# Kernel tuning notes

Hardware: AMD Instinct MI355X
Metric: run time of the kernel (lower is better)

The kernel has to match this reference:

```python
import jax, jax.numpy as jnp
import numpy as np

N = 120000
CIN = 64
C = 128
H = 8
FF = 1.0          # focusing_factor
EPS = 1e-4
BN_EPS = 1e-3
LN_EPS = 1e-3
GX, GY, GZ = 160, 160, 40  # voxel grid for generating realistic sparse coords


def _bn(x, g, b, m, v):
    # inference-mode BatchNorm1d
    return (x - m) * jax.lax.rsqrt(v + BN_EPS) * g + b


def _ln(x, g, b):
    mu = jnp.mean(x, axis=-1, keepdims=True)
    var = jnp.mean(jnp.square(x - mu), axis=-1, keepdims=True)
    return (x - mu) * jax.lax.rsqrt(var + LN_EPS) * g + b


def _l2(x):
    return jnp.sqrt(jnp.sum(jnp.square(x), axis=-1, keepdims=True))


def _forward(features, indices, nbr, W_pre, b_pre, g_pre, be_pre, m_pre, v_pre,
             Wp1, bp1, g_pe, be_pe, m_pe, v_pe, Wp2, bp2,
             W_qkv, b_qkv, scale_p, W_dwc, b_dwc, W_proj, b_proj, g_n1, b_n1):
    sp = _bn(features @ W_pre + b_pre, g_pre, be_pre, m_pre, v_pre)      # [N,C]
    xyz = indices[:, 1:].astype(sp.dtype)                                # [N,3]
    pe = jax.nn.relu(_bn(xyz @ Wp1 + bp1, g_pe, be_pe, m_pe, v_pe)) @ Wp2 + bp2
    qkv = (sp @ W_qkv + b_qkv).reshape(-1, 3, C)
    q, k, v = qkv[:, 0], qkv[:, 1], qkv[:, 2]
    k = k + pe
    # kernel feature map: ReLU + eps
    q = jax.nn.relu(q) + EPS
    k = jax.nn.relu(k) + EPS
    scale = jax.nn.softplus(scale_p)
    q = q / scale
    k = k / scale
    qn, kn = _l2(q), _l2(k)
    # power-law focusing (focusing_factor <= 6 branch)
    q = q ** FF
    k = k ** FF
    # L2 renormalization back to original norms
    q = q / _l2(q) * qn
    k = k / _l2(k) * kn
    d = C // H
    q = q.reshape(-1, H, d).transpose(1, 0, 2)   # [H,N,d]
    k = k.reshape(-1, H, d).transpose(1, 0, 2)
    v = v.reshape(-1, H, d).transpose(1, 0, 2)
    i = j = q.shape[1]
    z = 1.0 / (jnp.einsum('hic,hc->hi', q, k.sum(axis=1)) + EPS)         # [H,N]
    if i * j * (d + d) > d * d * (i + j):
        kv = jnp.einsum('hjc,hjd->hcd', k, v)                            # [H,d,d]
        x = jnp.einsum('hic,hcd->hid', q, kv) * z[..., None]
    else:
        qk = jnp.einsum('hic,hjc->hij', q, k)
        x = jnp.einsum('hij,hjd->hid', qk, v) * z[..., None]
    x = x.transpose(1, 0, 2).reshape(-1, C)                              # [N,C]
    v_full = v.transpose(1, 0, 2).reshape(-1, C)
    # SubMConv3d(C, C, 3) on v via precomputed neighbor table nbr [N,27] (-1 = absent)
    conv = jnp.zeros_like(x)
    nmax = v_full.shape[0] - 1
    for t in range(27):
        idx = nbr[:, t]
        g = jnp.where((idx >= 0)[:, None], v_full[jnp.clip(idx, 0, nmax)], 0.0)
        conv = conv + g @ W_dwc[t]
    conv = conv + b_dwc
    x = x + conv
    x = x @ W_proj + b_proj
    x = _ln(x + sp, g_n1, b_n1)
    return x


def setup_inputs() -> dict:
    rng = np.random.default_rng(0)
    total = GX * GY * GZ
    lin = rng.choice(total, size=N, replace=False)
    x = lin // (GY * GZ)
    rem = lin % (GY * GZ)
    y = rem // GZ
    z = rem % GZ
    dense = -np.ones(total, dtype=np.int32)
    dense[lin] = np.arange(N, dtype=np.int32)
    cols = []
    for dx in (-1, 0, 1):
        for dy in (-1, 0, 1):
            for dz in (-1, 0, 1):
                nx, ny, nz = x + dx, y + dy, z + dz
                valid = (nx >= 0) & (nx < GX) & (ny >= 0) & (ny < GY) & (nz >= 0) & (nz < GZ)
                nlin = np.clip(nx * GY * GZ + ny * GZ + nz, 0, total - 1)
                cols.append(np.where(valid, dense[nlin], -1).astype(np.int32))
    nbr = np.stack(cols, axis=1)
    indices = np.stack([np.zeros(N, dtype=np.int32), x.astype(np.int32),
                        y.astype(np.int32), z.astype(np.int32)], axis=1)
    key = jax.random.key(0)
    ks = jax.random.split(key, 10)
    rn = lambda k, shape, s=0.05: jax.random.normal(k, shape, jnp.float32) * s
    return {
        'features': jax.random.normal(ks[0], (N, CIN), jnp.float32),
        'indices': jnp.asarray(indices),
        'nbr': jnp.asarray(nbr),
        'W_pre': rn(ks[1], (CIN, C)), 'b_pre': jnp.zeros((C,), jnp.float32),
        'g_pre': jnp.ones((C,), jnp.float32), 'be_pre': jnp.zeros((C,), jnp.float32),
        'm_pre': jnp.zeros((C,), jnp.float32), 'v_pre': jnp.ones((C,), jnp.float32),
        'Wp1': rn(ks[2], (3, C)), 'bp1': jnp.zeros((C,), jnp.float32),
        'g_pe': jnp.ones((C,), jnp.float32), 'be_pe': jnp.zeros((C,), jnp.float32),
        'm_pe': jnp.zeros((C,), jnp.float32), 'v_pe': jnp.ones((C,), jnp.float32),
        'Wp2': rn(ks[3], (C, C)), 'bp2': jnp.zeros((C,), jnp.float32),
        'W_qkv': rn(ks[4], (C, 3 * C)), 'b_qkv': jnp.zeros((3 * C,), jnp.float32),
        'scale_p': rn(ks[5], (1, C), 0.5),
        'W_dwc': rn(ks[6], (27, C, C)), 'b_dwc': jnp.zeros((C,), jnp.float32),
        'W_proj': rn(ks[7], (C, C)), 'b_proj': jnp.zeros((C,), jnp.float32),
        'g_n1': jnp.ones((C,), jnp.float32), 'b_n1': jnp.zeros((C,), jnp.float32),
    }


def reference(features, indices, nbr, W_pre, b_pre, g_pre, be_pre, m_pre, v_pre,
              Wp1, bp1, g_pe, be_pe, m_pe, v_pe, Wp2, bp2,
              W_qkv, b_qkv, scale_p, W_dwc, b_dwc, W_proj, b_proj, g_n1, b_n1):
    return _forward(features, indices, nbr, W_pre, b_pre, g_pre, be_pre, m_pre, v_pre,
                    Wp1, bp1, g_pe, be_pe, m_pe, v_pe, Wp2, bp2,
                    W_qkv, b_qkv, scale_p, W_dwc, b_dwc, W_proj, b_proj, g_n1, b_n1)
```

## Files before the change

### kernel.cpp

```cpp
#include <hip/hip_runtime.h>
#include <math.h>

#define EPS 1e-4f
#define BN_EPS 1e-3f
#define LN_EPS 1e-3f

typedef float f32x4 __attribute__((ext_vector_type(4)));
typedef __bf16 bf16x8 __attribute__((ext_vector_type(8)));

__device__ __forceinline__ unsigned int bf16hi_rne(float v){
    unsigned int u = __float_as_uint(v);
    unsigned int r = u + 0x7FFFu + ((u >> 16) & 1u);
    return r & 0xFFFF0000u;
}
__device__ __forceinline__ unsigned int pack_hilo(float v){
    unsigned int hi = bf16hi_rne(v);
    float res = v - __uint_as_float(hi);
    unsigned int u2 = __float_as_uint(res);
    unsigned int r2 = u2 + 0x7FFFu + ((u2 >> 16) & 1u);
    return hi | (r2 >> 16);
}
__device__ __forceinline__ f32x4 mfma16(uint4 a, uint4 b, f32x4 c){
    union { uint4 u; bf16x8 v; } A, B;
    A.u = a; B.u = b;
    return __builtin_amdgcn_mfma_f32_16x16x32_bf16(A.v, B.v, c, 0, 0, 0);
}

__global__ __launch_bounds__(256) void k_pre(
    const float* __restrict__ feat, const float* __restrict__ W_pre,
    const float* __restrict__ b_pre, const float* __restrict__ g_pre,
    const float* __restrict__ be_pre, const float* __restrict__ m_pre,
    const float* __restrict__ v_pre, float* __restrict__ sp,
    float* __restrict__ accums)
{
    __shared__ __align__(16) float ft[16][64];
    int tid = threadIdx.x;
    int r0 = blockIdx.x * 16;
    if (blockIdx.x == 0){
        for (int i = tid; i < 2176; i += 256) accums[i] = 0.f;
    }
    {
        const float4* src = (const float4*)(feat + (size_t)r0 * 64);
        ((float4*)ft)[tid] = src[tid];
    }
    __syncthreads();
    int c = tid & 127;
    int rg = tid >> 7;
    float acc[8] = {0.f,0.f,0.f,0.f,0.f,0.f,0.f,0.f};
    #pragma unroll
    for (int k = 0; k < 64; k += 4){
        float w0 = W_pre[(k+0)*128 + c];
        float w1 = W_pre[(k+1)*128 + c];
        float w2 = W_pre[(k+2)*128 + c];
        float w3 = W_pre[(k+3)*128 + c];
        #pragma unroll
        for (int j = 0; j < 8; j++){
            float4 a = *(const float4*)&ft[rg*8 + j][k];
            acc[j] += a.x*w0 + a.y*w1 + a.z*w2 + a.w*w3;
        }
    }
    float aa = g_pre[c] * rsqrtf(v_pre[c] + BN_EPS);
    float cc = (b_pre[c] - m_pre[c]) * aa + be_pre[c];
    #pragma unroll
    for (int j = 0; j < 8; j++){
        size_t row = r0 + rg*8 + j;
        sp[row*128 + c] = acc[j]*aa + cc;
    }
}

__global__ __launch_bounds__(256) void k_wprep(
    const float* __restrict__ W, unsigned int* __restrict__ whl)
{
    int o = blockIdx.x*256 + threadIdx.x;
    if (o >= 27*128*128) return;
    int k = o & 127; int c = (o >> 7) & 127; int t = o >> 14;
    float v = W[(size_t)((t << 7) + k)*128 + c];
    whl[o] = pack_hilo(v);
}

__global__ __launch_bounds__(256) void k_qkv(
    const float* __restrict__ sp, const int* __restrict__ indices,
    const float* __restrict__ Wp1, const float* __restrict__ bp1,
    const float* __restrict__ g_pe, const float* __restrict__ be_pe,
    const float* __restrict__ m_pe, const float* __restrict__ v_pe,
    const float* __restrict__ Wp2, const float* __restrict__ bp2,
    const float* __restrict__ W_qkv, const float* __restrict__ b_qkv,
    const float* __restrict__ scale_p,
    float* __restrict__ qb, float* __restrict__ kb, unsigned int* __restrict__ vhl)
{
    __shared__ __align__(16) float spt[32][128];
    __shared__ __align__(16) float peh[32][128];
    __shared__ float xyzs[32][3];
    int tid = threadIdx.x;
    int r0 = blockIdx.x * 32;
    {
        const float4* src = (const float4*)(sp + (size_t)r0 * 128);
        float4* dst = (float4*)&spt[0][0];
        #pragma unroll
        for (int u = 0; u < 4; u++) dst[tid + 256*u] = src[tid + 256*u];
    }
    if (tid < 96){
        int r = tid / 3, d = tid % 3;
        xyzs[r][d] = (float)indices[(size_t)(r0 + r)*4 + 1 + d];
    }
    __syncthreads();
    #pragma unroll
    for (int u = 0; u < 16; u++){
        int oi = tid + 256*u;
        int r = oi >> 7, c = oi & 127;
        float dot = xyzs[r][0]*Wp1[c] + xyzs[r][1]*Wp1[128+c] + xyzs[r][2]*Wp1[256+c] + bp1[c];
        float aa = g_pe[c] * rsqrtf(v_pe[c] + BN_EPS);
        float t = (dot - m_pe[c])*aa + be_pe[c];
        peh[r][c] = fmaxf(t, 0.f);
    }
    __syncthreads();
    int c = tid & 127, rg = tid >> 7;
    float accq[16] = {0}, acck[16] = {0}, accv[16] = {0}, accp[16] = {0};
    for (int k = 0; k < 128; k += 4){
        float wq[4], wk[4], wv[4], wp[4];
        #pragma unroll
        for (int i = 0; i < 4; i++){
            wq[i] = W_qkv[(size_t)(k+i)*384 + c];
            wk[i] = W_qkv[(size_t)(k+i)*384 + 128 + c];
            wv[i] = W_qkv[(size_t)(k+i)*384 + 256 + c];
            wp[i] = Wp2[(k+i)*128 + c];
        }
        #pragma unroll
        for (int j = 0; j < 16; j++){
            float4 a = *(const float4*)&spt[rg*16 + j][k];
            accq[j] += a.x*wq[0] + a.y*wq[1] + a.z*wq[2] + a.w*wq[3];
            acck[j] += a.x*wk[0] + a.y*wk[1] + a.z*wk[2] + a.w*wk[3];
            accv[j] += a.x*wv[0] + a.y*wv[1] + a.z*wv[2] + a.w*wv[3];
            float4 p = *(const float4*)&peh[rg*16 + j][k];
            accp[j] += p.x*wp[0] + p.y*wp[1] + p.z*wp[2] + p.w*wp[3];
        }
    }
    float bq = b_qkv[c], bk = b_qkv[128 + c], bv = b_qkv[256 + c], bp = bp2[c];
    float sx = scale_p[c];
    float sc = (sx > 20.f) ? sx : log1pf(expf(sx));
    float inv = 1.f / sc;
    #pragma unroll
    for (int j = 0; j < 16; j++){
        size_t row = r0 + rg*16 + j;
        float pe = accp[j] + bp;
        float qv = (fmaxf(accq[j] + bq, 0.f) + EPS) * inv;
        float kv = (fmaxf(acck[j] + bk + pe, 0.f) + EPS) * inv;
        qb[row*128 + c] = qv;
        kb[row*128 + c] = kv;
        vhl[row*128 + c] = pack_hilo(accv[j] + bv);
    }
}

__global__ __launch_bounds__(256) void k_red(
    const float* __restrict__ kb, const unsigned int* __restrict__ vhl,
    float* __restrict__ ksum, float* __restrict__ kvm, int ntiles)
{
    __shared__ __align__(16) float kt[16][128];
    __shared__ __align__(16) unsigned int vt[16][128];
    int tid = threadIdx.x;
    int he = tid & 127, fh = tid >> 7;
    int h = he >> 4;
    float akv[8] = {0,0,0,0,0,0,0,0};
    float aks = 0.f;
    for (int ti = blockIdx.x; ti < ntiles; ti += gridDim.x){
        size_t base = (size_t)ti * 16 * 128;
        const float4* ks_ = (const float4*)(kb + base);
        const uint4* vs_ = (const uint4*)(vhl + base);
        float4* kd = (float4*)&kt[0][0];
        uint4* vd = (uint4*)&vt[0][0];
        __syncthreads();
        kd[tid] = ks_[tid]; kd[tid + 256] = ks_[tid + 256];
        vd[tid] = vs_[tid]; vd[tid + 256] = vs_[tid + 256];
        __syncthreads();
        #pragma unroll 4
        for (int r = 0; r < 16; r++){
            float kval = kt[r][he];
            const unsigned int* vr = &vt[r][h*16 + fh*8];
            #pragma unroll
            for (int j = 0; j < 8; j++){
                unsigned int p = vr[j];
                float vj = __uint_as_float(p & 0xFFFF0000u) + __uint_as_float(p << 16);
                akv[j] += kval * vj;
            }
            if (fh == 0) aks += kval;
        }
    }
    #pragma unroll
    for (int j = 0; j < 8; j++) atomicAdd(&kvm[he*16 + fh*8 + j], akv[j]);
    if (fh == 0) atomicAdd(&ksum[he], aks);
}

__global__ __launch_bounds__(256) void k_conv(
    const unsigned int* __restrict__ vhl, const int* __restrict__ nbr,
    const unsigned int* __restrict__ whl, const float* __restrict__ b_dwc,
    float* __restrict__ xb)
{
    __shared__ __align__(16) unsigned int vt[64*128];
    __shared__ int nbT[27*64];
    int tid = threadIdx.x;
    int r0 = blockIdx.x * 64;
    for (int i = tid; i < 27*64; i += 256){
        int t = i >> 6, r = i & 63;
        nbT[i] = nbr[(size_t)(r0 + r)*27 + t];
    }
    int lane = tid & 63;
    int w    = tid >> 6;
    int m    = lane & 15;
    int h    = lane >> 4;
    int sw   = m & 7;
    int tr   = tid >> 5, tc = tid & 31;
    int colbase = w * 32;

    f32x4 acc[4][2];
    #pragma unroll
    for (int rb = 0; rb < 4; rb++)
        #pragma unroll
        for (int cbi = 0; cbi < 2; cbi++)
            acc[rb][cbi] = (f32x4){0.f,0.f,0.f,0.f};

    const unsigned int* bbase0 = whl + ((size_t)(colbase      + m) << 7);
    const unsigned int* bbase1 = whl + ((size_t)(colbase + 16 + m) << 7);

    for (int t = 0; t < 27; t++){
        __syncthreads();
        #pragma unroll
        for (int s = 0; s < 8; s++){
            int r = tr + 8*s;
            int idx = nbT[t*64 + r];
            uint4 val = make_uint4(0u,0u,0u,0u);
            if (idx >= 0) val = *(const uint4*)&vhl[(size_t)idx*128 + tc*4];
            *(uint4*)&vt[r*128 + (((tc ^ (r & 7)) << 2))] = val;
        }
        __syncthreads();
        const unsigned int* bt0 = bbase0 + ((size_t)t << 14);
        const unsigned int* bt1 = bbase1 + ((size_t)t << 14);
        #pragma unroll
        for (int ks = 0; ks < 4; ks++){
            const unsigned int* bp0 = bt0 + ks*32 + h*8;
            const unsigned int* bp1 = bt1 + ks*32 + h*8;
            uint4 b00 = *(const uint4*)bp0;
            uint4 b01 = *(const uint4*)(bp0 + 4);
            uint4 b10 = *(const uint4*)bp1;
            uint4 b11 = *(const uint4*)(bp1 + 4);
            int G = ks*8 + h*2;
            int offA0 = ((G     ^ sw) << 2);
            int offA1 = (((G+1) ^ sw) << 2);
            uint4 aq[4][2];
            #pragma unroll
            for (int rb = 0; rb < 4; rb++){
                const unsigned int* ap = &vt[(rb*16 + m)*128];
                aq[rb][0] = *(const uint4*)&ap[offA0];
                aq[rb][1] = *(const uint4*)&ap[offA1];
            }
            uint4 ahi[4], alo[4];
            #pragma unroll
            for (int rb = 0; rb < 4; rb++){
                ahi[rb].x = __builtin_amdgcn_perm(aq[rb][0].y, aq[rb][0].x, 0x07060302u);
                ahi[rb].y = __builtin_amdgcn_perm(aq[rb][0].w, aq[rb][0].z, 0x07060302u);
                ahi[rb].z = __builtin_amdgcn_perm(aq[rb][1].y, aq[rb][1].x, 0x07060302u);
                ahi[rb].w = __builtin_amdgcn_perm(aq[rb][1].w, aq[rb][1].z, 0x07060302u);
                alo[rb].x = __builtin_amdgcn_perm(aq[rb][0].y, aq[rb][0].x, 0x05040100u);
                alo[rb].y = __builtin_amdgcn_perm(aq[rb][0].w, aq[rb][0].z, 0x05040100u);
                alo[rb].z = __builtin_amdgcn_perm(aq[rb][1].y, aq[rb][1].x, 0x05040100u);
                alo[rb].w = __builtin_amdgcn_perm(aq[rb][1].w, aq[rb][1].z, 0x05040100u);
            }
            {
                uint4 bhi, blo;
                bhi.x = __builtin_amdgcn_perm(b00.y, b00.x, 0x07060302u);
                bhi.y = __builtin_amdgcn_perm(b00.w, b00.z, 0x07060302u);
                bhi.z = __builtin_amdgcn_perm(b01.y, b01.x, 0x07060302u);
                bhi.w = __builtin_amdgcn_perm(b01.w, b01.z, 0x07060302u);
                blo.x = __builtin_amdgcn_perm(b00.y, b00.x, 0x05040100u);
                blo.y = __builtin_amdgcn_perm(b00.w, b00.z, 0x05040100u);
                blo.z = __builtin_amdgcn_perm(b01.y, b01.x, 0x05040100u);
                blo.w = __builtin_amdgcn_perm(b01.w, b01.z, 0x05040100u);
                #pragma unroll
                for (int rb = 0; rb < 4; rb++){
                    acc[rb][0] = mfma16(ahi[rb], bhi, acc[rb][0]);
                    acc[rb][0] = mfma16(alo[rb], bhi, acc[rb][0]);
                    acc[rb][0] = mfma16(ahi[rb], blo, acc[rb][0]);
                }
            }
            {
                uint4 bhi, blo;
                bhi.x = __builtin_amdgcn_perm(b10.y, b10.x, 0x07060302u);
                bhi.y = __builtin_amdgcn_perm(b10.w, b10.z, 0x07060302u);
                bhi.z = __builtin_amdgcn_perm(b11.y, b11.x, 0x07060302u);
                bhi.w = __builtin_amdgcn_perm(b11.w, b11.z, 0x07060302u);
                blo.x = __builtin_amdgcn_perm(b10.y, b10.x, 0x05040100u);
                blo.y = __builtin_amdgcn_perm(b10.w, b10.z, 0x05040100u);
                blo.z = __builtin_amdgcn_perm(b11.y, b11.x, 0x05040100u);
                blo.w = __builtin_amdgcn_perm(b11.w, b11.z, 0x05040100u);
                #pragma unroll
                for (int rb = 0; rb < 4; rb++){
                    acc[rb][1] = mfma16(ahi[rb], bhi, acc[rb][1]);
                    acc[rb][1] = mfma16(alo[rb], bhi, acc[rb][1]);
                    acc[rb][1] = mfma16(ahi[rb], blo, acc[rb][1]);
                }
            }
        }
    }
    #pragma unroll
    for (int cbi = 0; cbi < 2; cbi++){
        int col = colbase + cbi*16 + m;
        float bias = b_dwc[col];
        #pragma unroll
        for (int rb = 0; rb < 4; rb++){
            #pragma unroll
            for (int rr = 0; rr < 4; rr++){
                size_t row = (size_t)r0 + rb*16 + h*4 + rr;
                xb[row*128 + col] = acc[rb][cbi][rr] + bias;
            }
        }
    }
}

__global__ __launch_bounds__(256) void k_out(
    const float* __restrict__ xb, const float* __restrict__ qb,
    const float* __restrict__ ksum, const float* __restrict__ kvm,
    const float* __restrict__ W_proj, const float* __restrict__ b_proj,
    const float* __restrict__ sp, const float* __restrict__ g_n1,
    const float* __restrict__ b_n1, float* __restrict__ out)
{
    __shared__ __align__(16) float yt[16][128];
    __shared__ __align__(16) float qt[16][128];
    __shared__ float kvl[2048];
    __shared__ float ksl[128];
    int tid = threadIdx.x;
    int r0 = blockIdx.x * 16;
    {
        const float4* srcy = (const float4*)(xb + (size_t)r0 * 128);
        const float4* srcq = (const float4*)(qb + (size_t)r0 * 128);
        float4* dsty = (float4*)&yt[0][0];
        float4* dstq = (float4*)&qt[0][0];
        dsty[tid] = srcy[tid]; dsty[tid + 256] = srcy[tid + 256];
        dstq[tid] = srcq[tid]; dstq[tid + 256] = srcq[tid + 256];
    }
    #pragma unroll
    for (int u = 0; u < 8; u++) kvl[tid + 256*u] = kvm[tid + 256*u];
    if (tid < 128) ksl[tid] = ksum[tid];
    __syncthreads();

    int c2 = (tid & 63) * 2;
    int rg = tid >> 6;
    {
        int h = c2 >> 4, f0 = c2 & 15;
        float kv0[16], kv1[16], ks[16];
        #pragma unroll
        for (int e = 0; e < 16; e++){
            kv0[e] = kvl[(h*16 + e)*16 + f0];
            kv1[e] = kvl[(h*16 + e)*16 + f0 + 1];
            ks[e]  = ksl[h*16 + e];
        }
        float y[4][2];
        #pragma unroll
        for (int j = 0; j < 4; j++){
            int r = rg*4 + j;
            float zd = 0.f, x0 = 0.f, x1 = 0.f;
            #pragma unroll
            for (int e = 0; e < 16; e++){
                float qe = qt[r][h*16 + e];
                zd += qe * ks[e];
                x0 += qe * kv0[e];
                x1 += qe * kv1[e];
            }
            float iz = 1.f / (zd + EPS);
            y[j][0] = x0*iz + yt[r][c2];
            y[j][1] = x1*iz + yt[r][c2+1];
        }
        #pragma unroll
        for (int j = 0; j < 4; j++){
            yt[rg*4 + j][c2]     = y[j][0];
            yt[rg*4 + j][c2 + 1] = y[j][1];
        }
    }
    __syncthreads();
    float acc[4][2] = {{0,0},{0,0},{0,0},{0,0}};
    for (int k = 0; k < 128; k += 4){
        float2 w0 = *(const float2*)&W_proj[(k+0)*128 + c2];
        float2 w1 = *(const float2*)&W_proj[(k+1)*128 + c2];
        float2 w2 = *(const float2*)&W_proj[(k+2)*128 + c2];
        float2 w3 = *(const float2*)&W_proj[(k+3)*128 + c2];
        #pragma unroll
        for (int j = 0; j < 4; j++){
            float4 a = *(const float4*)&yt[rg*4 + j][k];
            acc[j][0] += a.x*w0.x + a.y*w1.x + a.z*w2.x + a.w*w3.x;
            acc[j][1] += a.x*w0.y + a.y*w1.y + a.z*w2.y + a.w*w3.y;
        }
    }
    float bp0 = b_proj[c2], bp1_ = b_proj[c2+1];
    float g0 = g_n1[c2], g1 = g_n1[c2+1], B0 = b_n1[c2], B1 = b_n1[c2+1];
    float z[4][2], s[4], ss[4];
    #pragma unroll
    for (int j = 0; j < 4; j++){
        size_t row = r0 + rg*4 + j;
        float2 spv = *(const float2*)&sp[row*128 + c2];
        float z0 = acc[j][0] + bp0 + spv.x;
        float z1 = acc[j][1] + bp1_ + spv.y;
        z[j][0] = z0; z[j][1] = z1;
        s[j] = z0 + z1; ss[j] = z0*z0 + z1*z1;
    }
    #pragma unroll
    for (int m = 1; m < 64; m <<= 1){
        #pragma unroll
        for (int j = 0; j < 4; j++){
            s[j]  += __shfl_xor(s[j],  m, 64);
            ss[j] += __shfl_xor(ss[j], m, 64);
        }
    }
    #pragma unroll
    for (int j = 0; j < 4; j++){
        size_t row = r0 + rg*4 + j;
        float mu = s[j] * (1.f/128.f);
        float var = ss[j] * (1.f/128.f) - mu*mu;
        float rstd = rsqrtf(var + LN_EPS);
        float2 o;
        o.x = (z[j][0] - mu)*rstd*g0 + B0;
        o.y = (z[j][1] - mu)*rstd*g1 + B1;
        *(float2*)&out[row*128 + c2] = o;
    }
}

extern "C" void kernel_launch(void* const* d_in, const int* in_sizes, int n_in,
                              void* d_out, int out_size, void* d_ws, size_t ws_size,
                              hipStream_t stream)
{
    const float* feat    = (const float*)d_in[0];
    const int*   indices = (const int*)  d_in[1];
    const int*   nbr     = (const int*)  d_in[2];
    const float* W_pre   = (const float*)d_in[3];
    const float* b_pre   = (const float*)d_in[4];
    const float* g_pre   = (const float*)d_in[5];
    const float* be_pre  = (const float*)d_in[6];
    const float* m_pre   = (const float*)d_in[7];
    const float* v_pre   = (const float*)d_in[8];
    const float* Wp1     = (const float*)d_in[9];
    const float* bp1     = (const float*)d_in[10];
    const float* g_pe    = (const float*)d_in[11];
    const float* be_pe   = (const float*)d_in[12];
    const float* m_pe    = (const float*)d_in[13];
    const float* v_pe    = (const float*)d_in[14];
    const float* Wp2     = (const float*)d_in[15];
    const float* bp2     = (const float*)d_in[16];
    const float* W_qkv   = (const float*)d_in[17];
    const float* b_qkv   = (const float*)d_in[18];
    const float* scale_p = (const float*)d_in[19];
    const float* W_dwc   = (const float*)d_in[20];
    const float* b_dwc   = (const float*)d_in[21];
    const float* W_proj  = (const float*)d_in[22];
    const float* b_proj  = (const float*)d_in[23];
    const float* g_n1    = (const float*)d_in[24];
    const float* b_n1    = (const float*)d_in[25];
    float* out = (float*)d_out;

    int N = in_sizes[0] / 64;
    size_t NC = (size_t)N * 128;
    float* ws   = (float*)d_ws;
    float* sp   = ws;
    float* qb   = ws + NC;
    float* kb   = ws + 2*NC;
    unsigned int* vhl = (unsigned int*)(ws + 3*NC);
    float* ksum = ws + 4*NC;
    float* kvm  = ksum + 128;
    unsigned int* whl = (unsigned int*)(ksum + 2176);
    float* xb   = kb;

    k_wprep<<<1728, 256, 0, stream>>>(W_dwc, whl);
    k_pre  <<<N/16, 256, 0, stream>>>(feat, W_pre, b_pre, g_pre, be_pre, m_pre, v_pre, sp, ksum);
    k_qkv  <<<N/32, 256, 0, stream>>>(sp, indices, Wp1, bp1, g_pe, be_pe, m_pe, v_pe,
                                      Wp2, bp2, W_qkv, b_qkv, scale_p, qb, kb, vhl);
    k_red  <<<256,  256, 0, stream>>>(kb, vhl, ksum, kvm, N/16);
    k_conv <<<N/64, 256, 0, stream>>>(vhl, nbr, whl, b_dwc, xb);
    k_out  <<<N/16, 256, 0, stream>>>(xb, qb, ksum, kvm, W_proj, b_proj, sp, g_n1, b_n1, out);
}
```

Measured before the change: 1.240 ms.

## Move QKV and positional-encoding GEMM onto split-bf16 MFMA

Replaces the scalar FP32 QKV/Wp2 projection in k_qkv with bf16 hi/lo split MFMA (three products per tile), using a new weight-prep kernel that packs W_qkv and Wp2 into hi/lo octets. The sp activations are now stored as packed hi/lo bf16 pairs so they can feed MFMA directly, and k_out unpacks them for the residual. Each wave handles one of q, k, v or pe, and pe is shared through LDS for the k epilogue. The goal is to remove the VALU-bound GEMM cost; the split-bf16 scheme trades some precision for this.

```diff
diff --git a/kernel.cpp b/kernel.cpp
--- a/kernel.cpp
+++ b/kernel.cpp
@@ -20,6 +20,9 @@
     unsigned int r2 = u2 + 0x7FFFu + ((u2 >> 16) & 1u);
     return hi | (r2 >> 16);
 }
+__device__ __forceinline__ float unpack_hilo(unsigned int p){
+    return __uint_as_float(p & 0xFFFF0000u) + __uint_as_float(p << 16);
+}
 __device__ __forceinline__ f32x4 mfma16(uint4 a, uint4 b, f32x4 c){
     union { uint4 u; bf16x8 v; } A, B;
     A.u = a; B.u = b;
@@ -30,7 +33,7 @@
     const float* __restrict__ feat, const float* __restrict__ W_pre,
     const float* __restrict__ b_pre, const float* __restrict__ g_pre,
     const float* __restrict__ be_pre, const float* __restrict__ m_pre,
-    const float* __restrict__ v_pre, float* __restrict__ sp,
+    const float* __restrict__ v_pre, unsigned int* __restrict__ sphl,
     float* __restrict__ accums)
 {
     __shared__ __align__(16) float ft[16][64];
@@ -64,7 +67,7 @@
     #pragma unroll
     for (int j = 0; j < 8; j++){
         size_t row = r0 + rg*8 + j;
-        sp[row*128 + c] = acc[j]*aa + cc;
+        sphl[row*128 + c] = pack_hilo(acc[j]*aa + cc);
     }
 }
 
@@ -78,30 +81,65 @@
     whl[o] = pack_hilo(v);
 }
 
+__global__ __launch_bounds__(256) void k_wprep2(
+    const float* __restrict__ Wqkv, const float* __restrict__ Wp2,
+    uint4* __restrict__ qwhl)
+{
+    int o = blockIdx.x*256 + threadIdx.x;
+    if (o >= 8192) return;
+    int koct = o & 15, col = o >> 4;
+    float v[8];
+    #pragma unroll
+    for (int j = 0; j < 8; j++){
+        int k = koct*8 + j;
+        v[j] = (col < 384) ? Wqkv[(size_t)k*384 + col] : Wp2[(size_t)k*128 + (col - 384)];
+    }
+    unsigned int hi[4], lo[4];
+    #pragma unroll
+    for (int j2 = 0; j2 < 4; j2++){
+        float a = v[2*j2], b = v[2*j2+1];
+        unsigned int ha = bf16hi_rne(a), hb = bf16hi_rne(b);
+        float ra = a - __uint_as_float(ha);
+        float rb = b - __uint_as_float(hb);
+        hi[j2] = (ha >> 16) | (hb & 0xFFFF0000u);
+        lo[j2] = (bf16hi_rne(ra) >> 16) | (bf16hi_rne(rb) & 0xFFFF0000u);
+    }
+    qwhl[o]        = make_uint4(hi[0],hi[1],hi[2],hi[3]);
+    qwhl[8192 + o] = make_uint4(lo[0],lo[1],lo[2],lo[3]);
+}
+
 __global__ __launch_bounds__(256) void k_qkv(
-    const float* __restrict__ sp, const int* __restrict__ indices,
+    const unsigned int* __restrict__ sphl, const int* __restrict__ indices,
     const float* __restrict__ Wp1, const float* __restrict__ bp1,
     const float* __restrict__ g_pe, const float* __restrict__ be_pe,
     const float* __restrict__ m_pe, const float* __restrict__ v_pe,
-    const float* __restrict__ Wp2, const float* __restrict__ bp2,
-    const float* __restrict__ W_qkv, const float* __restrict__ b_qkv,
-    const float* __restrict__ scale_p,
+    const float* __restrict__ bp2, const uint4* __restrict__ qwhl,
+    const float* __restrict__ b_qkv, const float* __restrict__ scale_p,
     float* __restrict__ qb, float* __restrict__ kb, unsigned int* __restrict__ vhl)
 {
-    __shared__ __align__(16) float spt[32][128];
-    __shared__ __align__(16) float peh[32][128];
+    __shared__ __align__(16) unsigned int At[2][32*132];
+    __shared__ float peout[32*128];
+    __shared__ float invs[128];
     __shared__ float xyzs[32][3];
     int tid = threadIdx.x;
     int r0 = blockIdx.x * 32;
     {
-        const float4* src = (const float4*)(sp + (size_t)r0 * 128);
-        float4* dst = (float4*)&spt[0][0];
-        #pragma unroll
-        for (int u = 0; u < 4; u++) dst[tid + 256*u] = src[tid + 256*u];
+        const uint4* src = (const uint4*)(sphl + (size_t)r0*128);
+        #pragma unroll
+        for (int u = 0; u < 4; u++){
+            int i = tid + 256*u;
+            int r = i >> 5, cq = i & 31;
+            *(uint4*)&At[0][r*132 + cq*4] = src[i];
+        }
     }
     if (tid < 96){
         int r = tid / 3, d = tid % 3;
         xyzs[r][d] = (float)indices[(size_t)(r0 + r)*4 + 1 + d];
+    }
+    if (tid < 128){
+        float sx = scale_p[tid];
+        float sc = (sx > 20.f) ? sx : log1pf(expf(sx));
+        invs[tid] = 1.f / sc;
     }
     __syncthreads();
     #pragma unroll
@@ -111,43 +149,120 @@
         float dot = xyzs[r][0]*Wp1[c] + xyzs[r][1]*Wp1[128+c] + xyzs[r][2]*Wp1[256+c] + bp1[c];
         float aa = g_pe[c] * rsqrtf(v_pe[c] + BN_EPS);
         float t = (dot - m_pe[c])*aa + be_pe[c];
-        peh[r][c] = fmaxf(t, 0.f);
+        At[1][r*132 + c] = pack_hilo(fmaxf(t, 0.f));
     }
     __syncthreads();
-    int c = tid & 127, rg = tid >> 7;
-    float accq[16] = {0}, acck[16] = {0}, accv[16] = {0}, accp[16] = {0};
-    for (int k = 0; k < 128; k += 4){
-        float wq[4], wk[4], wv[4], wp[4];
-        #pragma unroll
-        for (int i = 0; i < 4; i++){
-            wq[i] = W_qkv[(size_t)(k+i)*384 + c];
-            wk[i] = W_qkv[(size_t)(k+i)*384 + 128 + c];
-            wv[i] = W_qkv[(size_t)(k+i)*384 + 256 + c];
-            wp[i] = Wp2[(k+i)*128 + c];
-        }
-        #pragma unroll
-        for (int j = 0; j < 16; j++){
-            float4 a = *(const float4*)&spt[rg*16 + j][k];
-            accq[j] += a.x*wq[0] + a.y*wq[1] + a.z*wq[2] + a.w*wq[3];
-            acck[j] += a.x*wk[0] + a.y*wk[1] + a.z*wk[2] + a.w*wk[3];
-            accv[j] += a.x*wv[0] + a.y*wv[1] + a.z*wv[2] + a.w*wv[3];
-            float4 p = *(const float4*)&peh[rg*16 + j][k];
-            accp[j] += p.x*wp[0] + p.y*wp[1] + p.z*wp[2] + p.w*wp[3];
-        }
-    }
-    float bq = b_qkv[c], bk = b_qkv[128 + c], bv = b_qkv[256 + c], bp = bp2[c];
-    float sx = scale_p[c];
-    float sc = (sx > 20.f) ? sx : log1pf(expf(sx));
-    float inv = 1.f / sc;
-    #pragma unroll
-    for (int j = 0; j < 16; j++){
-        size_t row = r0 + rg*16 + j;
-        float pe = accp[j] + bp;
-        float qv = (fmaxf(accq[j] + bq, 0.f) + EPS) * inv;
-        float kv = (fmaxf(acck[j] + bk + pe, 0.f) + EPS) * inv;
-        qb[row*128 + c] = qv;
-        kb[row*128 + c] = kv;
-        vhl[row*128 + c] = pack_hilo(accv[j] + bv);
+
+    int lane = tid & 63;
+    int w = tid >> 6;
+    int m = lane & 15, kq = lane >> 4;
+    const unsigned int* A = &At[w == 3 ? 1 : 0][0];
+
+    uint4 ahi[2][4], alo[2][4];
+    #pragma unroll
+    for (int rt = 0; rt < 2; rt++){
+        #pragma unroll
+        for (int ks = 0; ks < 4; ks++){
+            const unsigned int* ap = &A[(rt*16 + m)*132 + ks*32 + kq*8];
+            uint4 a0 = *(const uint4*)ap;
+            uint4 a1 = *(const uint4*)(ap + 4);
+            uint4 h, l;
+            h.x = __builtin_amdgcn_perm(a0.y, a0.x, 0x07060302u);
+            h.y = __builtin_amdgcn_perm(a0.w, a0.z, 0x07060302u);
+            h.z = __builtin_amdgcn_perm(a1.y, a1.x, 0x07060302u);
+            h.w = __builtin_amdgcn_perm(a1.w, a1.z, 0x07060302u);
+            l.x = __builtin_amdgcn_perm(a0.y, a0.x, 0x05040100u);
+            l.y = __builtin_amdgcn_perm(a0.w, a0.z, 0x05040100u);
+            l.z = __builtin_amdgcn_perm(a1.y, a1.x, 0x05040100u);
+            l.w = __builtin_amdgcn_perm(a1.w, a1.z, 0x05040100u);
+            ahi[rt][ks] = h; alo[rt][ks] = l;
+        }
+    }
+
+    f32x4 acc[2][8];
+    #pragma unroll
+    for (int rt = 0; rt < 2; rt++)
+        #pragma unroll
+        for (int ct = 0; ct < 8; ct++)
+            acc[rt][ct] = (f32x4){0.f,0.f,0.f,0.f};
+
+    int colg = w * 128;
+    #pragma unroll
+    for (int ct = 0; ct < 8; ct++){
+        #pragma unroll
+        for (int ks = 0; ks < 4; ks++){
+            int bu = (colg + ct*16 + m)*16 + ks*4 + kq;
+            uint4 bhi = qwhl[bu];
+            uint4 blo = qwhl[8192 + bu];
+            #pragma unroll
+            for (int rt = 0; rt < 2; rt++){
+                acc[rt][ct] = mfma16(ahi[rt][ks], bhi, acc[rt][ct]);
+                acc[rt][ct] = mfma16(alo[rt][ks], bhi, acc[rt][ct]);
+                acc[rt][ct] = mfma16(ahi[rt][ks], blo, acc[rt][ct]);
+            }
+        }
+    }
+
+    if (w == 3){
+        #pragma unroll
+        for (int ct = 0; ct < 8; ct++){
+            int col = ct*16 + m;
+            float bp = bp2[col];
+            #pragma unroll
+            for (int rt = 0; rt < 2; rt++){
+                #pragma unroll
+                for (int reg = 0; reg < 4; reg++){
+                    int row = rt*16 + kq*4 + reg;
+                    peout[row*128 + col] = acc[rt][ct][reg] + bp;
+                }
+            }
+        }
+    }
+    __syncthreads();
+    if (w == 0){
+        #pragma unroll
+        for (int ct = 0; ct < 8; ct++){
+            int col = ct*16 + m;
+            float bq = b_qkv[col], inv = invs[col];
+            #pragma unroll
+            for (int rt = 0; rt < 2; rt++){
+                #pragma unroll
+                for (int reg = 0; reg < 4; reg++){
+                    int row = rt*16 + kq*4 + reg;
+                    float v = acc[rt][ct][reg] + bq;
+                    qb[(size_t)(r0 + row)*128 + col] = (fmaxf(v, 0.f) + EPS) * inv;
+                }
+            }
+        }
+    } else if (w == 1){
+        #pragma unroll
+        for (int ct = 0; ct < 8; ct++){
+            int col = ct*16 + m;
+            float bk = b_qkv[128 + col], inv = invs[col];
+            #pragma unroll
+            for (int rt = 0; rt < 2; rt++){
+                #pragma unroll
+                for (int reg = 0; reg < 4; reg++){
+                    int row = rt*16 + kq*4 + reg;
+                    float v = acc[rt][ct][reg] + bk + peout[row*128 + col];
+                    kb[(size_t)(r0 + row)*128 + col] = (fmaxf(v, 0.f) + EPS) * inv;
+                }
+            }
+        }
+    } else if (w == 2){
+        #pragma unroll
+        for (int ct = 0; ct < 8; ct++){
+            int col = ct*16 + m;
+            float bv = b_qkv[256 + col];
+            #pragma unroll
+            for (int rt = 0; rt < 2; rt++){
+                #pragma unroll
+                for (int reg = 0; reg < 4; reg++){
+                    int row = rt*16 + kq*4 + reg;
+                    vhl[(size_t)(r0 + row)*128 + col] = pack_hilo(acc[rt][ct][reg] + bv);
+                }
+            }
+        }
     }
 }
 
@@ -178,9 +293,7 @@
             const unsigned int* vr = &vt[r][h*16 + fh*8];
             #pragma unroll
             for (int j = 0; j < 8; j++){
-                unsigned int p = vr[j];
-                float vj = __uint_as_float(p & 0xFFFF0000u) + __uint_as_float(p << 16);
-                akv[j] += kval * vj;
+                akv[j] += kval * unpack_hilo(vr[j]);
             }
             if (fh == 0) aks += kval;
         }
@@ -304,12 +417,13 @@
     for (int cbi = 0; cbi < 2; cbi++){
         int col = colbase + cbi*16 + m;
         float bias = b_dwc[col];
+        f32x4* a = (cbi == 0) ? nullptr : nullptr; (void)a;
         #pragma unroll
         for (int rb = 0; rb < 4; rb++){
             #pragma unroll
             for (int rr = 0; rr < 4; rr++){
                 size_t row = (size_t)r0 + rb*16 + h*4 + rr;
-                xb[row*128 + col] = acc[rb][cbi][rr] + bias;
+                xb[row*128 + col] = ((cbi == 0) ? acc[rb][0][rr] : acc[rb][1][rr]) + bias;
             }
         }
     }
@@ -319,7 +433,7 @@
     const float* __restrict__ xb, const float* __restrict__ qb,
     const float* __restrict__ ksum, const float* __restrict__ kvm,
     const float* __restrict__ W_proj, const float* __restrict__ b_proj,
-    const float* __restrict__ sp, const float* __restrict__ g_n1,
+    const unsigned int* __restrict__ sphl, const float* __restrict__ g_n1,
     const float* __restrict__ b_n1, float* __restrict__ out)
 {
     __shared__ __align__(16) float yt[16][128];
@@ -394,9 +508,9 @@
     #pragma unroll
     for (int j = 0; j < 4; j++){
         size_t row = r0 + rg*4 + j;
-        float2 spv = *(const float2*)&sp[row*128 + c2];
-        float z0 = acc[j][0] + bp0 + spv.x;
-        float z1 = acc[j][1] + bp1_ + spv.y;
+        uint2 spv = *(const uint2*)&sphl[row*128 + c2];
+        float z0 = acc[j][0] + bp0 + unpack_hilo(spv.x);
+        float z1 = acc[j][1] + bp1_ + unpack_hilo(spv.y);
         z[j][0] = z0; z[j][1] = z1;
         s[j] = z0 + z1; ss[j] = z0*z0 + z1*z1;
     }
@@ -456,20 +570,22 @@
     int N = in_sizes[0] / 64;
     size_t NC = (size_t)N * 128;
     float* ws   = (float*)d_ws;
-    float* sp   = ws;
+    unsigned int* sphl = (unsigned int*)ws;
     float* qb   = ws + NC;
     float* kb   = ws + 2*NC;
     unsigned int* vhl = (unsigned int*)(ws + 3*NC);
     float* ksum = ws + 4*NC;
     float* kvm  = ksum + 128;
-    unsigned int* whl = (unsigned int*)(ksum + 2176);
+    unsigned int* whl = (unsigned int*)(ksum + 2560);
+    uint4* qwhl = (uint4*)(whl + 27*128*128);
     float* xb   = kb;
 
-    k_wprep<<<1728, 256, 0, stream>>>(W_dwc, whl);
-    k_pre  <<<N/16, 256, 0, stream>>>(feat, W_pre, b_pre, g_pre, be_pre, m_pre, v_pre, sp, ksum);
-    k_qkv  <<<N/32, 256, 0, stream>>>(sp, indices, Wp1, bp1, g_pe, be_pe, m_pe, v_pe,
-                                      Wp2, bp2, W_qkv, b_qkv, scale_p, qb, kb, vhl);
-    k_red  <<<256,  256, 0, stream>>>(kb, vhl, ksum, kvm, N/16);
-    k_conv <<<N/64, 256, 0, stream>>>(vhl, nbr, whl, b_dwc, xb);
-    k_out  <<<N/16, 256, 0, stream>>>(xb, qb, ksum, kvm, W_proj, b_proj, sp, g_n1, b_n1, out);
-}
+    k_wprep <<<1728, 256, 0, stream>>>(W_dwc, whl);
+    k_wprep2<<<32,   256, 0, stream>>>(W_qkv, Wp2, qwhl);
+    k_pre   <<<N/16, 256, 0, stream>>>(feat, W_pre, b_pre, g_pre, be_pre, m_pre, v_pre, sphl, ksum);
+    k_qkv   <<<N/32, 256, 0, stream>>>(sphl, indices, Wp1, bp1, g_pe, be_pe, m_pe, v_pe,
+                                       bp2, qwhl, b_qkv, scale_p, qb, kb, vhl);
+    k_red   <<<256,  256, 0, stream>>>(kb, vhl, ksum, kvm, N/16);
+    k_conv  <<<N/64, 256, 0, stream>>>(vhl, nbr, whl, b_dwc, xb);
+    k_out   <<<N/16, 256, 0, stream>>>(xb, qb, ksum, kvm, W_proj, b_proj, sphl, g_n1, b_n1, out);
+}
```

New measurement: 1.096 ms. 11.6% less time.
